# Kernel optimization log

Measured on AMD Instinct MI355X. Metric: run time of the kernel, lower is better.

## Reference

```python
import jax, jax.numpy as jnp
import numpy as np

EPS = 1e-5


def conv1x1(x, w, b):
    # x: [b,c,h,w], w: [o,c], b: [o] -> [b,o,h,w]  (1x1 conv == channel matmul)
    return jnp.einsum('bchw,oc->bohw', x, w) + b[None, :, None, None]


def nor_mean_std(x):
    # instance norm over spatial dims (torch calc_mean_std uses unbiased var)
    mean = jnp.mean(x, axis=(2, 3), keepdims=True)
    var = jnp.var(x, axis=(2, 3), keepdims=True, ddof=1)
    return (x - mean) / jnp.sqrt(var + EPS)


def nor_mean(x):
    mean = jnp.mean(x, axis=(2, 3), keepdims=True)
    return x - mean, mean


def net(x, w1, b1, w2, b2):
    return conv1x1(jax.nn.relu(conv1x1(x, w1, b1)), w2, b2)


def setup_inputs() -> dict:
    key = jax.random.key(0)
    ks = jax.random.split(key, 8)
    B, C, H, W = 8, 256, 128, 128
    return {
        'content': jax.random.normal(ks[0], (B, C, H, W), jnp.float32),
        'style': jax.random.normal(ks[1], (B, C, H, W), jnp.float32),
        'w1': jax.random.normal(ks[2], (128, 256), jnp.float32) * 0.05,
        'b1': jax.random.normal(ks[3], (128,), jnp.float32) * 0.05,
        'w2': jax.random.normal(ks[4], (32, 128), jnp.float32) * 0.05,
        'b2': jax.random.normal(ks[5], (32,), jnp.float32) * 0.05,
        'wu': jax.random.normal(ks[6], (256, 32), jnp.float32) * 0.05,
        'bu': jax.random.normal(ks[7], (256,), jnp.float32) * 0.05,
    }


def reference(content, style, w1, b1, w2, b2, wu, bu):
    cF_nor = nor_mean_std(content)
    sF_nor, smean = nor_mean(style)
    cF = net(cF_nor, w1, b1, w2, b2)          # [b,32,h,w]
    sF = net(sF_nor, w1, b1, w2, b2)          # [b,32,h,w]
    b, c, h, w = cF.shape
    hw = h * w
    sf = sF.reshape(b, c, hw)
    # channel covariance: [b,32,32]
    s_cov = jnp.einsum('bcn,bdn->bcd', sf, sf) / hw
    s_cov = jax.nn.softmax(s_cov, axis=-1) * (c ** -0.5)
    gF = jnp.einsum('bcd,bdn->bcn', s_cov, cF.reshape(b, c, hw)).reshape(b, c, h, w)
    gF = conv1x1(gF, wu, bu)                  # [b,256,h,w]
    return gF + smean + content
```

## Files before the change

### kernel.cpp

```cpp
#include <hip/hip_runtime.h>

#define HW 16384
#define C_IN 256
#define C_MID 128
#define C_OUT 32
#define EPSF 1e-5f

typedef __bf16 bf16x8 __attribute__((ext_vector_type(8)));
typedef __bf16 bf16x4 __attribute__((ext_vector_type(4)));
typedef float f32x4 __attribute__((ext_vector_type(4)));

__device__ __forceinline__ bf16x4 cvt4(f32x4 v) {
    bf16x4 r;
    r[0] = (__bf16)v[0]; r[1] = (__bf16)v[1];
    r[2] = (__bf16)v[2]; r[3] = (__bf16)v[3];
    return r;
}

template <int MODE>
__global__ __launch_bounds__(512) void k_stats8(const float* __restrict__ content,
                                                const float* __restrict__ style,
                                                float* __restrict__ cmean,
                                                float* __restrict__ crstd,
                                                float* __restrict__ smean,
                                                __bf16* __restrict__ cbf,
                                                __bf16* __restrict__ sbf) {
    const int bc = blockIdx.x;
    const int t = threadIdx.x;
    const f32x4* cp = (const f32x4*)(content + (size_t)bc * HW);
    const f32x4* sp = (const f32x4*)(style + (size_t)bc * HW);
    const int phase = (bc * 257) & 4095;

    int idx[8];
    #pragma unroll
    for (int i = 0; i < 8; ++i) idx[i] = (phase + t + i * 512) & 4095;

    f32x4 c[8], s[8];
    #pragma unroll
    for (int i = 0; i < 8; ++i)
        c[i] = (MODE == 1) ? __builtin_nontemporal_load(cp + idx[i]) : cp[idx[i]];
    #pragma unroll
    for (int i = 0; i < 8; ++i)
        s[i] = __builtin_nontemporal_load(sp + idx[i]);
    asm volatile("" ::
        "v"(c[0]), "v"(c[1]), "v"(c[2]), "v"(c[3]), "v"(c[4]), "v"(c[5]), "v"(c[6]), "v"(c[7]),
        "v"(s[0]), "v"(s[1]), "v"(s[2]), "v"(s[3]), "v"(s[4]), "v"(s[5]), "v"(s[6]), "v"(s[7]));

    if constexpr (MODE == 1) {
        bf16x4* cb = (bf16x4*)(cbf + (size_t)bc * HW);
        bf16x4* sb = (bf16x4*)(sbf + (size_t)bc * HW);
        #pragma unroll
        for (int i = 0; i < 8; ++i) {
            cb[idx[i]] = cvt4(c[i]);
            sb[idx[i]] = cvt4(s[i]);
        }
    }

    float cs, cq, ss;
    {
        f32x4 a01 = c[0] + c[1], a23 = c[2] + c[3], a45 = c[4] + c[5], a67 = c[6] + c[7];
        f32x4 a = (a01 + a23) + (a45 + a67);
        cs = (a[0] + a[1]) + (a[2] + a[3]);
        f32x4 q01 = c[0]*c[0] + c[1]*c[1], q23 = c[2]*c[2] + c[3]*c[3];
        f32x4 q45 = c[4]*c[4] + c[5]*c[5], q67 = c[6]*c[6] + c[7]*c[7];
        f32x4 q = (q01 + q23) + (q45 + q67);
        cq = (q[0] + q[1]) + (q[2] + q[3]);
        f32x4 b01 = s[0] + s[1], b23 = s[2] + s[3], b45 = s[4] + s[5], b67 = s[6] + s[7];
        f32x4 bsum = (b01 + b23) + (b45 + b67);
        ss = (bsum[0] + bsum[1]) + (bsum[2] + bsum[3]);
    }

    #pragma unroll
    for (int d = 32; d > 0; d >>= 1) {
        cs += __shfl_xor(cs, d, 64);
        cq += __shfl_xor(cq, d, 64);
        ss += __shfl_xor(ss, d, 64);
    }
    __shared__ float rs[8], rq[8], rss[8];
    const int wv = t >> 6;
    if ((t & 63) == 0) { rs[wv] = cs; rq[wv] = cq; rss[wv] = ss; }
    __syncthreads();
    if (t == 0) {
        float S = 0.f, Q = 0.f, SS = 0.f;
        #pragma unroll
        for (int i = 0; i < 8; ++i) { S += rs[i]; Q += rq[i]; SS += rss[i]; }
        float n = (float)HW;
        float var = (Q - S * S / n) / (n - 1.f);
        cmean[bc] = S / n;
        crstd[bc] = 1.f / sqrtf(var + EPSF);
        smean[bc] = SS / n;
    }
}

__global__ __launch_bounds__(256) void k_wprep(const float* __restrict__ w1,
                                               const float* __restrict__ b1,
                                               const float* __restrict__ cmean,
                                               const float* __restrict__ crstd,
                                               const float* __restrict__ smean,
                                               __bf16* __restrict__ W1c,
                                               float* __restrict__ bias1c,
                                               __bf16* __restrict__ W1s,
                                               float* __restrict__ bias1s) {
    int o = blockIdx.x, b = blockIdx.y, t = threadIdx.x;
    float w = w1[o * 256 + t];
    float r = crstd[b * 256 + t];
    float wc = w * r;
    W1c[((size_t)(b * 128 + o)) * 256 + t] = (__bf16)wc;
    if (b == 0) W1s[o * 256 + t] = (__bf16)w;
    float pc = wc * cmean[b * 256 + t];
    float ps = w * smean[b * 256 + t];
    __shared__ float rA[256], rB[256];
    rA[t] = pc; rB[t] = ps;
    __syncthreads();
    for (int off = 128; off > 0; off >>= 1) {
        if (t < off) { rA[t] += rA[t + off]; rB[t] += rB[t + off]; }
        __syncthreads();
    }
    if (t == 0) {
        bias1c[b * 128 + o] = b1[o] - rA[0];
        bias1s[b * 128 + o] = b1[o] - rB[0];
    }
}

__global__ __launch_bounds__(256) void k_w2prep(const float* __restrict__ w2,
                                                __bf16* __restrict__ W2b) {
    int i = blockIdx.x * 256 + threadIdx.x;
    if (i < 4096) W2b[i] = (__bf16)w2[i];
}

template <bool NT>
__device__ __forceinline__ float ld_f32(const float* p) {
    if constexpr (NT) return __builtin_nontemporal_load(p);
    else return *p;
}

template <bool NT_X>
__global__ __launch_bounds__(256) void k_net_mfma(const float* __restrict__ x,
                                                  const __bf16* __restrict__ W1,
                                                  const float* __restrict__ bias1,
                                                  const __bf16* __restrict__ W2,
                                                  const float* __restrict__ b2,
                                                  float* __restrict__ outF,
                                                  int w1_per_batch) {
    __shared__ __bf16 Xl[64 * 256];
    __shared__ __bf16 Tl[64 * 128];
    const int tid = threadIdx.x;
    const int l = tid & 63, wv = tid >> 6;
    const int lr = l & 15, g = l >> 4;
    const int sw = (lr & 7) << 4;
    const int p0 = blockIdx.x * 64;
    const int b = blockIdx.y;
    const float* xb = x + (size_t)b * C_IN * HW;

    {
        const int p = wv * 16 + lr;
        const float* xp = xb + p0 + p;
        char* row = (char*)&Xl[p * 256];
        #pragma unroll 4
        for (int cc = 0; cc < 16; ++cc) {
            const int c = cc * 16 + g * 4;
            float f0 = ld_f32<NT_X>(xp + (size_t)(c + 0) * HW);
            float f1 = ld_f32<NT_X>(xp + (size_t)(c + 1) * HW);
            float f2 = ld_f32<NT_X>(xp + (size_t)(c + 2) * HW);
            float f3 = ld_f32<NT_X>(xp + (size_t)(c + 3) * HW);
            bf16x4 v;
            v[0] = (__bf16)f0; v[1] = (__bf16)f1; v[2] = (__bf16)f2; v[3] = (__bf16)f3;
            *(bf16x4*)(row + ((c * 2) ^ sw)) = v;
        }
    }
    __syncthreads();

    const f32x4 zero4 = {0.f, 0.f, 0.f, 0.f};
    f32x4 acc[2][4];
    #pragma unroll
    for (int mt = 0; mt < 2; ++mt)
        #pragma unroll
        for (int nt = 0; nt < 4; ++nt) acc[mt][nt] = zero4;

    const __bf16* W1b = W1 + (w1_per_batch ? ((size_t)b << 15) : 0);
    const __bf16* wrow0 = W1b + (size_t)(wv * 32 + lr) * 256 + g * 8;
    const __bf16* wrow1 = wrow0 + 16 * 256;

    #pragma unroll
    for (int kt = 0; kt < 8; ++kt) {
        bf16x8 a0 = *(const bf16x8*)(wrow0 + kt * 32);
        bf16x8 a1 = *(const bf16x8*)(wrow1 + kt * 32);
        #pragma unroll
        for (int nt = 0; nt < 4; ++nt) {
            const char* xrow = (const char*)&Xl[(nt * 16 + lr) * 256];
            bf16x8 bfr = *(const bf16x8*)(xrow + (((kt * 32 + g * 8) * 2) ^ sw));
            acc[0][nt] = __builtin_amdgcn_mfma_f32_16x16x32_bf16(a0, bfr, acc[0][nt], 0, 0, 0);
            acc[1][nt] = __builtin_amdgcn_mfma_f32_16x16x32_bf16(a1, bfr, acc[1][nt], 0, 0, 0);
        }
    }

    float4 bia[2];
    bia[0] = *(const float4*)&bias1[b * 128 + wv * 32 + g * 4];
    bia[1] = *(const float4*)&bias1[b * 128 + wv * 32 + 16 + g * 4];
    #pragma unroll
    for (int mt = 0; mt < 2; ++mt) {
        #pragma unroll
        for (int nt = 0; nt < 4; ++nt) {
            const int p = nt * 16 + lr;
            char* trow = (char*)&Tl[p * 128];
            const int ob = (wv * 32 + mt * 16 + g * 4) * 2;
            bf16x4 tv;
            tv[0] = (__bf16)fmaxf(acc[mt][nt][0] + bia[mt].x, 0.f);
            tv[1] = (__bf16)fmaxf(acc[mt][nt][1] + bia[mt].y, 0.f);
            tv[2] = (__bf16)fmaxf(acc[mt][nt][2] + bia[mt].z, 0.f);
            tv[3] = (__bf16)fmaxf(acc[mt][nt][3] + bia[mt].w, 0.f);
            *(bf16x4*)(trow + (ob ^ sw)) = tv;
        }
    }
    __syncthreads();

    f32x4 acc2[2];
    acc2[0] = zero4; acc2[1] = zero4;
    const int p = wv * 16 + lr;
    const char* trow = (const char*)&Tl[p * 128];
    const __bf16* w2r0 = W2 + (size_t)lr * 128 + g * 8;
    const __bf16* w2r1 = w2r0 + 16 * 128;
    #pragma unroll
    for (int kt = 0; kt < 4; ++kt) {
        bf16x8 bfr = *(const bf16x8*)(trow + (((kt * 32 + g * 8) * 2) ^ sw));
        bf16x8 a0 = *(const bf16x8*)(w2r0 + kt * 32);
        bf16x8 a1 = *(const bf16x8*)(w2r1 + kt * 32);
        acc2[0] = __builtin_amdgcn_mfma_f32_16x16x32_bf16(a0, bfr, acc2[0], 0, 0, 0);
        acc2[1] = __builtin_amdgcn_mfma_f32_16x16x32_bf16(a1, bfr, acc2[1], 0, 0, 0);
    }
    float4 bb0 = *(const float4*)&b2[g * 4];
    float4 bb1 = *(const float4*)&b2[16 + g * 4];
    float* ob = outF + (size_t)b * C_OUT * HW + p0 + p;
    const int o0 = g * 4;
    ob[(size_t)(o0 + 0) * HW] = acc2[0][0] + bb0.x;
    ob[(size_t)(o0 + 1) * HW] = acc2[0][1] + bb0.y;
    ob[(size_t)(o0 + 2) * HW] = acc2[0][2] + bb0.z;
    ob[(size_t)(o0 + 3) * HW] = acc2[0][3] + bb0.w;
    ob[(size_t)(16 + o0 + 0) * HW] = acc2[1][0] + bb1.x;
    ob[(size_t)(16 + o0 + 1) * HW] = acc2[1][1] + bb1.y;
    ob[(size_t)(16 + o0 + 2) * HW] = acc2[1][2] + bb1.z;
    ob[(size_t)(16 + o0 + 3) * HW] = acc2[1][3] + bb1.w;
}

__global__ __launch_bounds__(256) void k_net_mfma_bf(const __bf16* __restrict__ x,
                                                     const __bf16* __restrict__ W1,
                                                     const float* __restrict__ bias1,
                                                     const __bf16* __restrict__ W2,
                                                     const float* __restrict__ b2,
                                                     float* __restrict__ outF,
                                                     int w1_per_batch) {
    __shared__ __bf16 Xl[64 * 256];
    __shared__ __bf16 Tl[64 * 128];
    const int tid = threadIdx.x;
    const int l = tid & 63, wv = tid >> 6;
    const int lr = l & 15, g = l >> 4;
    const int sw = (lr & 7) << 4;
    const int p0 = blockIdx.x * 64;
    const int b = blockIdx.y;
    const __bf16* xb = x + (size_t)b * C_IN * HW;

    {
        const int p = wv * 16 + lr;
        const __bf16* xp = xb + p0 + p;
        char* row = (char*)&Xl[p * 256];
        #pragma unroll 4
        for (int cc = 0; cc < 16; ++cc) {
            const int c = cc * 16 + g * 4;
            bf16x4 v;
            v[0] = xp[(size_t)(c + 0) * HW];
            v[1] = xp[(size_t)(c + 1) * HW];
            v[2] = xp[(size_t)(c + 2) * HW];
            v[3] = xp[(size_t)(c + 3) * HW];
            *(bf16x4*)(row + ((c * 2) ^ sw)) = v;
        }
    }
    __syncthreads();

    const f32x4 zero4 = {0.f, 0.f, 0.f, 0.f};
    f32x4 acc[2][4];
    #pragma unroll
    for (int mt = 0; mt < 2; ++mt)
        #pragma unroll
        for (int nt = 0; nt < 4; ++nt) acc[mt][nt] = zero4;

    const __bf16* W1b = W1 + (w1_per_batch ? ((size_t)b << 15) : 0);
    const __bf16* wrow0 = W1b + (size_t)(wv * 32 + lr) * 256 + g * 8;
    const __bf16* wrow1 = wrow0 + 16 * 256;

    #pragma unroll
    for (int kt = 0; kt < 8; ++kt) {
        bf16x8 a0 = *(const bf16x8*)(wrow0 + kt * 32);
        bf16x8 a1 = *(const bf16x8*)(wrow1 + kt * 32);
        #pragma unroll
        for (int nt = 0; nt < 4; ++nt) {
            const char* xrow = (const char*)&Xl[(nt * 16 + lr) * 256];
            bf16x8 bfr = *(const bf16x8*)(xrow + (((kt * 32 + g * 8) * 2) ^ sw));
            acc[0][nt] = __builtin_amdgcn_mfma_f32_16x16x32_bf16(a0, bfr, acc[0][nt], 0, 0, 0);
            acc[1][nt] = __builtin_amdgcn_mfma_f32_16x16x32_bf16(a1, bfr, acc[1][nt], 0, 0, 0);
        }
    }

    float4 bia[2];
    bia[0] = *(const float4*)&bias1[b * 128 + wv * 32 + g * 4];
    bia[1] = *(const float4*)&bias1[b * 128 + wv * 32 + 16 + g * 4];
    #pragma unroll
    for (int mt = 0; mt < 2; ++mt) {
        #pragma unroll
        for (int nt = 0; nt < 4; ++nt) {
            const int p = nt * 16 + lr;
            char* trow = (char*)&Tl[p * 128];
            const int ob = (wv * 32 + mt * 16 + g * 4) * 2;
            bf16x4 tv;
            tv[0] = (__bf16)fmaxf(acc[mt][nt][0] + bia[mt].x, 0.f);
            tv[1] = (__bf16)fmaxf(acc[mt][nt][1] + bia[mt].y, 0.f);
            tv[2] = (__bf16)fmaxf(acc[mt][nt][2] + bia[mt].z, 0.f);
            tv[3] = (__bf16)fmaxf(acc[mt][nt][3] + bia[mt].w, 0.f);
            *(bf16x4*)(trow + (ob ^ sw)) = tv;
        }
    }
    __syncthreads();

    f32x4 acc2[2];
    acc2[0] = zero4; acc2[1] = zero4;
    const int p = wv * 16 + lr;
    const char* trow = (const char*)&Tl[p * 128];
    const __bf16* w2r0 = W2 + (size_t)lr * 128 + g * 8;
    const __bf16* w2r1 = w2r0 + 16 * 128;
    #pragma unroll
    for (int kt = 0; kt < 4; ++kt) {
        bf16x8 bfr = *(const bf16x8*)(trow + (((kt * 32 + g * 8) * 2) ^ sw));
        bf16x8 a0 = *(const bf16x8*)(w2r0 + kt * 32);
        bf16x8 a1 = *(const bf16x8*)(w2r1 + kt * 32);
        acc2[0] = __builtin_amdgcn_mfma_f32_16x16x32_bf16(a0, bfr, acc2[0], 0, 0, 0);
        acc2[1] = __builtin_amdgcn_mfma_f32_16x16x32_bf16(a1, bfr, acc2[1], 0, 0, 0);
    }
    float4 bb0 = *(const float4*)&b2[g * 4];
    float4 bb1 = *(const float4*)&b2[16 + g * 4];
    float* ob = outF + (size_t)b * C_OUT * HW + p0 + p;
    const int o0 = g * 4;
    ob[(size_t)(o0 + 0) * HW] = acc2[0][0] + bb0.x;
    ob[(size_t)(o0 + 1) * HW] = acc2[0][1] + bb0.y;
    ob[(size_t)(o0 + 2) * HW] = acc2[0][2] + bb0.z;
    ob[(size_t)(o0 + 3) * HW] = acc2[0][3] + bb0.w;
    ob[(size_t)(16 + o0 + 0) * HW] = acc2[1][0] + bb1.x;
    ob[(size_t)(16 + o0 + 1) * HW] = acc2[1][1] + bb1.y;
    ob[(size_t)(16 + o0 + 2) * HW] = acc2[1][2] + bb1.z;
    ob[(size_t)(16 + o0 + 3) * HW] = acc2[1][3] + bb1.w;
}

__global__ __launch_bounds__(256) void k_gram(const float* __restrict__ sF,
                                              float* __restrict__ partial) {
    __shared__ float sS[32 * 257];
    int b = blockIdx.y, sl = blockIdx.x;
    int t = threadIdx.x;
    const float* base = sF + (size_t)b * C_OUT * HW + sl * 1024;
    int i = t >> 3, jb = (t & 7) * 4;
    float acc[4] = {0.f, 0.f, 0.f, 0.f};
    for (int ch = 0; ch < 4; ++ch) {
        __syncthreads();
        #pragma unroll
        for (int r = 0; r < 32; ++r)
            sS[r * 257 + t] = base[(size_t)r * HW + ch * 256 + t];
        __syncthreads();
        for (int n = 0; n < 256; ++n) {
            float si = sS[i * 257 + n];
            #pragma unroll
            for (int q = 0; q < 4; ++q)
                acc[q] = fmaf(si, sS[(jb + q) * 257 + n], acc[q]);
        }
    }
    float* dst = partial + ((size_t)(b * 16 + sl)) * 1024 + t * 4;
    #pragma unroll
    for (int q = 0; q < 4; ++q) dst[q] = acc[q];
}

__global__ __launch_bounds__(1024) void k_softmax(const float* __restrict__ partial,
                                                  float* __restrict__ scov) {
    int b = blockIdx.x;
    int j = threadIdx.x, i = threadIdx.y;
    float v = 0.f;
    #pragma unroll
    for (int s = 0; s < 16; ++s)
        v += partial[((size_t)(b * 16 + s)) * 1024 + i * 32 + j];
    v *= (1.f / (float)HW);
    float m = v;
    #pragma unroll
    for (int d = 16; d > 0; d >>= 1) m = fmaxf(m, __shfl_xor(m, d, 32));
    float e = expf(v - m);
    float sum = e;
    #pragma unroll
    for (int d = 16; d > 0; d >>= 1) sum += __shfl_xor(sum, d, 32);
    scov[(size_t)b * 1024 + i * 32 + j] = e / sum * 0.17677669529663687f;
}

template <bool CONTENT_BF16>
__global__ __launch_bounds__(256) void k_final(const float* __restrict__ cF,
                                               const float* __restrict__ scov,
                                               const float* __restrict__ wu,
                                               const float* __restrict__ bu,
                                               const float* __restrict__ smean,
                                               const float* __restrict__ content,
                                               const __bf16* __restrict__ cbf,
                                               float* __restrict__ out) {
    __shared__ float sCov[1024];
    __shared__ float sC[32 * 64];
    __shared__ float sG[32 * 64];
    __shared__ float sWu[32 * 260];
    int t = threadIdx.x;
    int p0 = blockIdx.x * 64;
    int b = blockIdx.y;
    #pragma unroll
    for (int q = 0; q < 4; ++q) sCov[t + 256 * q] = scov[(size_t)b * 1024 + t + 256 * q];
    {
        int p = t & 63, rb = t >> 6;
        #pragma unroll
        for (int pass = 0; pass < 8; ++pass) {
            int r = pass * 4 + rb;
            sC[r * 64 + p] = cF[(size_t)b * C_OUT * HW + (size_t)r * HW + p0 + p];
        }
    }
    {
        int k = t & 31, ob = t >> 5;
        #pragma unroll
        for (int pass = 0; pass < 32; ++pass) {
            int o = pass * 8 + ob;
            sWu[k * 260 + o] = wu[o * 32 + k];
        }
    }
    __syncthreads();
    {
        int gp = t & 63, gib = (t >> 6) * 8;
        #pragma unroll
        for (int rr = 0; rr < 8; ++rr) {
            int gi = gib + rr;
            float a = 0.f;
            #pragma unroll
            for (int k = 0; k < 32; ++k)
                a = fmaf(sCov[gi * 32 + k], sC[k * 64 + gp], a);
            sG[gi * 64 + gp] = a;
        }
    }
    __syncthreads();
    int tx = t & 7, ty = t >> 3;
    float acc[8][8];
    #pragma unroll
    for (int i = 0; i < 8; ++i)
        #pragma unroll
        for (int j = 0; j < 8; ++j) acc[i][j] = 0.f;
    #pragma unroll 4
    for (int k = 0; k < 32; ++k) {
        float4 a4a = *(const float4*)&sWu[k * 260 + ty * 8];
        float4 a4b = *(const float4*)&sWu[k * 260 + ty * 8 + 4];
        float4 b4a = *(const float4*)&sG[k * 64 + tx * 8];
        float4 b4b = *(const float4*)&sG[k * 64 + tx * 8 + 4];
        float a[8] = {a4a.x, a4a.y, a4a.z, a4a.w, a4b.x, a4b.y, a4b.z, a4b.w};
        float bb[8] = {b4a.x, b4a.y, b4a.z, b4a.w, b4b.x, b4b.y, b4b.z, b4b.w};
        #pragma unroll
        for (int i = 0; i < 8; ++i)
            #pragma unroll
            for (int j = 0; j < 8; ++j)
                acc[i][j] = fmaf(a[i], bb[j], acc[i][j]);
    }
    #pragma unroll
    for (int i = 0; i < 8; ++i) {
        int o = ty * 8 + i;
        float add = bu[o] + smean[b * 256 + o];
        float* dst = out + (size_t)b * C_IN * HW + (size_t)o * HW + p0 + tx * 8;
        float cv[8];
        if constexpr (CONTENT_BF16) {
            const __bf16* csrc = cbf + (size_t)b * C_IN * HW + (size_t)o * HW + p0 + tx * 8;
            bf16x8 cvv = *(const bf16x8*)csrc;
            #pragma unroll
            for (int q = 0; q < 8; ++q) cv[q] = (float)cvv[q];
        } else {
            const float* csrc = content + (size_t)b * C_IN * HW + (size_t)o * HW + p0 + tx * 8;
            float4 c0 = *(const float4*)csrc;
            float4 c1 = *(const float4*)(csrc + 4);
            cv[0] = c0.x; cv[1] = c0.y; cv[2] = c0.z; cv[3] = c0.w;
            cv[4] = c1.x; cv[5] = c1.y; cv[6] = c1.z; cv[7] = c1.w;
        }
        f32x4 r0 = {acc[i][0] + add + cv[0], acc[i][1] + add + cv[1],
                    acc[i][2] + add + cv[2], acc[i][3] + add + cv[3]};
        f32x4 r1 = {acc[i][4] + add + cv[4], acc[i][5] + add + cv[5],
                    acc[i][6] + add + cv[6], acc[i][7] + add + cv[7]};
        __builtin_nontemporal_store(r0, (f32x4*)dst);
        __builtin_nontemporal_store(r1, (f32x4*)(dst + 4));
    }
}

extern "C" void kernel_launch(void* const* d_in, const int* in_sizes, int n_in,
                              void* d_out, int out_size, void* d_ws, size_t ws_size,
                              hipStream_t stream) {
    const float* content = (const float*)d_in[0];
    const float* style   = (const float*)d_in[1];
    const float* w1      = (const float*)d_in[2];
    const float* b1      = (const float*)d_in[3];
    const float* w2      = (const float*)d_in[4];
    const float* b2      = (const float*)d_in[5];
    const float* wu      = (const float*)d_in[6];
    const float* bu      = (const float*)d_in[7];
    float* out = (float*)d_out;
    float* ws  = (float*)d_ws;

    const size_t NEED = 42240000ull * sizeof(float);
    if (ws_size >= NEED) {
        float* cmean   = ws;
        float* crstd   = ws + 2048;
        float* smean   = ws + 4096;
        float* scov    = ws + 6144;
        float* bias1c  = ws + 14336;
        float* bias1s  = ws + 15360;
        __bf16* W2b    = (__bf16*)(ws + 16384);
        __bf16* W1s    = (__bf16*)(ws + 18432);
        __bf16* W1c    = (__bf16*)(ws + 34816);
        float* partial = ws + 165888;
        float* cF      = ws + 296960;
        float* sF      = cF + 4194304;
        __bf16* cbf    = (__bf16*)(ws + 8685568);
        __bf16* sbf    = (__bf16*)(ws + 8685568 + 16777216);

        k_stats8<1><<<dim3(2048), 512, 0, stream>>>(content, style, cmean, crstd, smean, cbf, sbf);
        k_wprep<<<dim3(128, 8), 256, 0, stream>>>(w1, b1, cmean, crstd, smean,
                                                  W1c, bias1c, W1s, bias1s);
        k_w2prep<<<dim3(16), 256, 0, stream>>>(w2, W2b);
        k_net_mfma_bf<<<dim3(256, 8), 256, 0, stream>>>(cbf, W1c, bias1c, W2b, b2, cF, 1);
        k_net_mfma_bf<<<dim3(256, 8), 256, 0, stream>>>(sbf, W1s, bias1s, W2b, b2, sF, 0);
        k_gram<<<dim3(16, 8), 256, 0, stream>>>(sF, partial);
        k_softmax<<<dim3(8), dim3(32, 32), 0, stream>>>(partial, scov);
        k_final<true><<<dim3(256, 8), 256, 0, stream>>>(cF, scov, wu, bu, smean,
                                                        content, cbf, out);
    } else {
        float* cmean   = ws;
        float* crstd   = ws + 2048;
        float* smean   = ws + 4096;
        float* scov    = ws + 6144;
        __bf16* W2b    = (__bf16*)(ws + 6144);
        float* bias1c  = ws + 8192;
        float* bias1s  = ws + 9216;
        float* partial = ws + 14336;
        __bf16* W1c    = (__bf16*)(ws + 14336);
        __bf16* W1s    = (__bf16*)(ws + 145408);
        float* cF      = ws + 161792;
        float* sF      = cF + 4194304;

        k_stats8<0><<<dim3(2048), 512, 0, stream>>>(content, style, cmean, crstd, smean,
                                                    nullptr, nullptr);
        k_wprep<<<dim3(128, 8), 256, 0, stream>>>(w1, b1, cmean, crstd, smean,
                                                  W1c, bias1c, W1s, bias1s);
        k_w2prep<<<dim3(16), 256, 0, stream>>>(w2, W2b);
        k_net_mfma<false><<<dim3(256, 8), 256, 0, stream>>>(content, W1c, bias1c, W2b, b2, cF, 1);
        k_net_mfma<true><<<dim3(256, 8), 256, 0, stream>>>(style, W1s, bias1s, W2b, b2, sF, 0);
        k_gram<<<dim3(16, 8), 256, 0, stream>>>(sF, partial);
        k_softmax<<<dim3(8), dim3(32, 32), 0, stream>>>(partial, scov);
        k_final<false><<<dim3(256, 8), 256, 0, stream>>>(cF, scov, wu, bu, smean,
                                                         content, nullptr, out);
    }
}
```

Measured before the change: 246.3 us.

## Drop bf16 content copy, read fp32 content directly, fold w2 prep into wprep

The stats kernel no longer writes a bf16 copy of content; only style is converted to bf16. The content net pass reads fp32 content directly (hoping for cache hits after stats), and the final kernel reads fp32 content for the residual instead of the bf16 copy, which also removes the bf16 rounding of the residual. The separate w2 conversion kernel is merged into the weight-prep kernel. The final kernel reads wu directly from global/cache instead of staging it in shared memory. This trades a 32MB write for extra fp32 reads.

```diff
diff --git a/kernel.cpp b/kernel.cpp
--- a/kernel.cpp
+++ b/kernel.cpp
@@ -17,13 +17,11 @@
     return r;
 }
 
-template <int MODE>
-__global__ __launch_bounds__(512) void k_stats8(const float* __restrict__ content,
+__global__ __launch_bounds__(512) void k_stats9(const float* __restrict__ content,
                                                 const float* __restrict__ style,
                                                 float* __restrict__ cmean,
                                                 float* __restrict__ crstd,
                                                 float* __restrict__ smean,
-                                                __bf16* __restrict__ cbf,
                                                 __bf16* __restrict__ sbf) {
     const int bc = blockIdx.x;
     const int t = threadIdx.x;
@@ -37,23 +35,17 @@
 
     f32x4 c[8], s[8];
     #pragma unroll
-    for (int i = 0; i < 8; ++i)
-        c[i] = (MODE == 1) ? __builtin_nontemporal_load(cp + idx[i]) : cp[idx[i]];
-    #pragma unroll
-    for (int i = 0; i < 8; ++i)
-        s[i] = __builtin_nontemporal_load(sp + idx[i]);
+    for (int i = 0; i < 8; ++i) c[i] = cp[idx[i]];
+    #pragma unroll
+    for (int i = 0; i < 8; ++i) s[i] = __builtin_nontemporal_load(sp + idx[i]);
     asm volatile("" ::
         "v"(c[0]), "v"(c[1]), "v"(c[2]), "v"(c[3]), "v"(c[4]), "v"(c[5]), "v"(c[6]), "v"(c[7]),
         "v"(s[0]), "v"(s[1]), "v"(s[2]), "v"(s[3]), "v"(s[4]), "v"(s[5]), "v"(s[6]), "v"(s[7]));
 
-    if constexpr (MODE == 1) {
-        bf16x4* cb = (bf16x4*)(cbf + (size_t)bc * HW);
+    {
         bf16x4* sb = (bf16x4*)(sbf + (size_t)bc * HW);
         #pragma unroll
-        for (int i = 0; i < 8; ++i) {
-            cb[idx[i]] = cvt4(c[i]);
-            sb[idx[i]] = cvt4(s[i]);
-        }
+        for (int i = 0; i < 8; ++i) sb[idx[i]] = cvt4(s[i]);
     }
 
     float cs, cq, ss;
@@ -92,21 +84,26 @@
     }
 }
 
-__global__ __launch_bounds__(256) void k_wprep(const float* __restrict__ w1,
-                                               const float* __restrict__ b1,
-                                               const float* __restrict__ cmean,
-                                               const float* __restrict__ crstd,
-                                               const float* __restrict__ smean,
-                                               __bf16* __restrict__ W1c,
-                                               float* __restrict__ bias1c,
-                                               __bf16* __restrict__ W1s,
-                                               float* __restrict__ bias1s) {
+__global__ __launch_bounds__(256) void k_wprep2(const float* __restrict__ w1,
+                                                const float* __restrict__ b1,
+                                                const float* __restrict__ w2,
+                                                const float* __restrict__ cmean,
+                                                const float* __restrict__ crstd,
+                                                const float* __restrict__ smean,
+                                                __bf16* __restrict__ W1c,
+                                                float* __restrict__ bias1c,
+                                                __bf16* __restrict__ W1s,
+                                                float* __restrict__ bias1s,
+                                                __bf16* __restrict__ W2b) {
     int o = blockIdx.x, b = blockIdx.y, t = threadIdx.x;
     float w = w1[o * 256 + t];
     float r = crstd[b * 256 + t];
     float wc = w * r;
     W1c[((size_t)(b * 128 + o)) * 256 + t] = (__bf16)wc;
-    if (b == 0) W1s[o * 256 + t] = (__bf16)w;
+    if (b == 0) {
+        W1s[o * 256 + t] = (__bf16)w;
+        if (t < 32) W2b[o * 32 + t] = (__bf16)w2[o * 32 + t];
+    }
     float pc = wc * cmean[b * 256 + t];
     float ps = w * smean[b * 256 + t];
     __shared__ float rA[256], rB[256];
@@ -122,19 +119,6 @@
     }
 }
 
-__global__ __launch_bounds__(256) void k_w2prep(const float* __restrict__ w2,
-                                                __bf16* __restrict__ W2b) {
-    int i = blockIdx.x * 256 + threadIdx.x;
-    if (i < 4096) W2b[i] = (__bf16)w2[i];
-}
-
-template <bool NT>
-__device__ __forceinline__ float ld_f32(const float* p) {
-    if constexpr (NT) return __builtin_nontemporal_load(p);
-    else return *p;
-}
-
-template <bool NT_X>
 __global__ __launch_bounds__(256) void k_net_mfma(const float* __restrict__ x,
                                                   const __bf16* __restrict__ W1,
                                                   const float* __restrict__ bias1,
@@ -159,10 +143,10 @@
         #pragma unroll 4
         for (int cc = 0; cc < 16; ++cc) {
             const int c = cc * 16 + g * 4;
-            float f0 = ld_f32<NT_X>(xp + (size_t)(c + 0) * HW);
-            float f1 = ld_f32<NT_X>(xp + (size_t)(c + 1) * HW);
-            float f2 = ld_f32<NT_X>(xp + (size_t)(c + 2) * HW);
-            float f3 = ld_f32<NT_X>(xp + (size_t)(c + 3) * HW);
+            float f0 = xp[(size_t)(c + 0) * HW];
+            float f1 = xp[(size_t)(c + 1) * HW];
+            float f2 = xp[(size_t)(c + 2) * HW];
+            float f3 = xp[(size_t)(c + 3) * HW];
             bf16x4 v;
             v[0] = (__bf16)f0; v[1] = (__bf16)f1; v[2] = (__bf16)f2; v[3] = (__bf16)f3;
             *(bf16x4*)(row + ((c * 2) ^ sw)) = v;
@@ -393,19 +377,16 @@
     scov[(size_t)b * 1024 + i * 32 + j] = e / sum * 0.17677669529663687f;
 }
 
-template <bool CONTENT_BF16>
-__global__ __launch_bounds__(256) void k_final(const float* __restrict__ cF,
-                                               const float* __restrict__ scov,
-                                               const float* __restrict__ wu,
-                                               const float* __restrict__ bu,
-                                               const float* __restrict__ smean,
-                                               const float* __restrict__ content,
-                                               const __bf16* __restrict__ cbf,
-                                               float* __restrict__ out) {
+__global__ __launch_bounds__(256) void k_final2(const float* __restrict__ cF,
+                                                const float* __restrict__ scov,
+                                                const float* __restrict__ wu,
+                                                const float* __restrict__ bu,
+                                                const float* __restrict__ smean,
+                                                const float* __restrict__ content,
+                                                float* __restrict__ out) {
     __shared__ float sCov[1024];
     __shared__ float sC[32 * 64];
     __shared__ float sG[32 * 64];
-    __shared__ float sWu[32 * 260];
     int t = threadIdx.x;
     int p0 = blockIdx.x * 64;
     int b = blockIdx.y;
@@ -417,14 +398,6 @@
         for (int pass = 0; pass < 8; ++pass) {
             int r = pass * 4 + rb;
             sC[r * 64 + p] = cF[(size_t)b * C_OUT * HW + (size_t)r * HW + p0 + p];
-        }
-    }
-    {
-        int k = t & 31, ob = t >> 5;
-        #pragma unroll
-        for (int pass = 0; pass < 32; ++pass) {
-            int o = pass * 8 + ob;
-            sWu[k * 260 + o] = wu[o * 32 + k];
         }
     }
     __syncthreads();
@@ -442,6 +415,7 @@
     }
     __syncthreads();
     int tx = t & 7, ty = t >> 3;
+    const float* wurow = wu + (size_t)(ty * 8) * 32;
     float acc[8][8];
     #pragma unroll
     for (int i = 0; i < 8; ++i)
@@ -449,11 +423,11 @@
         for (int j = 0; j < 8; ++j) acc[i][j] = 0.f;
     #pragma unroll 4
     for (int k = 0; k < 32; ++k) {
-        float4 a4a = *(const float4*)&sWu[k * 260 + ty * 8];
-        float4 a4b = *(const float4*)&sWu[k * 260 + ty * 8 + 4];
+        float a[8];
+        #pragma unroll
+        for (int i = 0; i < 8; ++i) a[i] = wurow[i * 32 + k];
         float4 b4a = *(const float4*)&sG[k * 64 + tx * 8];
         float4 b4b = *(const float4*)&sG[k * 64 + tx * 8 + 4];
-        float a[8] = {a4a.x, a4a.y, a4a.z, a4a.w, a4b.x, a4b.y, a4b.z, a4b.w};
         float bb[8] = {b4a.x, b4a.y, b4a.z, b4a.w, b4b.x, b4b.y, b4b.z, b4b.w};
         #pragma unroll
         for (int i = 0; i < 8; ++i)
@@ -465,24 +439,14 @@
     for (int i = 0; i < 8; ++i) {
         int o = ty * 8 + i;
         float add = bu[o] + smean[b * 256 + o];
+        const float* csrc = content + (size_t)b * C_IN * HW + (size_t)o * HW + p0 + tx * 8;
         float* dst = out + (size_t)b * C_IN * HW + (size_t)o * HW + p0 + tx * 8;
-        float cv[8];
-        if constexpr (CONTENT_BF16) {
-            const __bf16* csrc = cbf + (size_t)b * C_IN * HW + (size_t)o * HW + p0 + tx * 8;
-            bf16x8 cvv = *(const bf16x8*)csrc;
-            #pragma unroll
-            for (int q = 0; q < 8; ++q) cv[q] = (float)cvv[q];
-        } else {
-            const float* csrc = content + (size_t)b * C_IN * HW + (size_t)o * HW + p0 + tx * 8;
-            float4 c0 = *(const float4*)csrc;
-            float4 c1 = *(const float4*)(csrc + 4);
-            cv[0] = c0.x; cv[1] = c0.y; cv[2] = c0.z; cv[3] = c0.w;
-            cv[4] = c1.x; cv[5] = c1.y; cv[6] = c1.z; cv[7] = c1.w;
-        }
-        f32x4 r0 = {acc[i][0] + add + cv[0], acc[i][1] + add + cv[1],
-                    acc[i][2] + add + cv[2], acc[i][3] + add + cv[3]};
-        f32x4 r1 = {acc[i][4] + add + cv[4], acc[i][5] + add + cv[5],
-                    acc[i][6] + add + cv[6], acc[i][7] + add + cv[7]};
+        float4 c0 = *(const float4*)csrc;
+        float4 c1 = *(const float4*)(csrc + 4);
+        f32x4 r0 = {acc[i][0] + add + c0.x, acc[i][1] + add + c0.y,
+                    acc[i][2] + add + c0.z, acc[i][3] + add + c0.w};
+        f32x4 r1 = {acc[i][4] + add + c1.x, acc[i][5] + add + c1.y,
+                    acc[i][6] + add + c1.z, acc[i][7] + add + c1.w};
         __builtin_nontemporal_store(r0, (f32x4*)dst);
         __builtin_nontemporal_store(r1, (f32x4*)(dst + 4));
     }
@@ -502,57 +466,26 @@
     float* out = (float*)d_out;
     float* ws  = (float*)d_ws;
 
-    const size_t NEED = 42240000ull * sizeof(float);
-    if (ws_size >= NEED) {
-        float* cmean   = ws;
-        float* crstd   = ws + 2048;
-        float* smean   = ws + 4096;
-        float* scov    = ws + 6144;
-        float* bias1c  = ws + 14336;
-        float* bias1s  = ws + 15360;
-        __bf16* W2b    = (__bf16*)(ws + 16384);
-        __bf16* W1s    = (__bf16*)(ws + 18432);
-        __bf16* W1c    = (__bf16*)(ws + 34816);
-        float* partial = ws + 165888;
-        float* cF      = ws + 296960;
-        float* sF      = cF + 4194304;
-        __bf16* cbf    = (__bf16*)(ws + 8685568);
-        __bf16* sbf    = (__bf16*)(ws + 8685568 + 16777216);
-
-        k_stats8<1><<<dim3(2048), 512, 0, stream>>>(content, style, cmean, crstd, smean, cbf, sbf);
-        k_wprep<<<dim3(128, 8), 256, 0, stream>>>(w1, b1, cmean, crstd, smean,
-                                                  W1c, bias1c, W1s, bias1s);
-        k_w2prep<<<dim3(16), 256, 0, stream>>>(w2, W2b);
-        k_net_mfma_bf<<<dim3(256, 8), 256, 0, stream>>>(cbf, W1c, bias1c, W2b, b2, cF, 1);
-        k_net_mfma_bf<<<dim3(256, 8), 256, 0, stream>>>(sbf, W1s, bias1s, W2b, b2, sF, 0);
-        k_gram<<<dim3(16, 8), 256, 0, stream>>>(sF, partial);
-        k_softmax<<<dim3(8), dim3(32, 32), 0, stream>>>(partial, scov);
-        k_final<true><<<dim3(256, 8), 256, 0, stream>>>(cF, scov, wu, bu, smean,
-                                                        content, cbf, out);
-    } else {
-        float* cmean   = ws;
-        float* crstd   = ws + 2048;
-        float* smean   = ws + 4096;
-        float* scov    = ws + 6144;
-        __bf16* W2b    = (__bf16*)(ws + 6144);
-        float* bias1c  = ws + 8192;
-        float* bias1s  = ws + 9216;
-        float* partial = ws + 14336;
-        __bf16* W1c    = (__bf16*)(ws + 14336);
-        __bf16* W1s    = (__bf16*)(ws + 145408);
-        float* cF      = ws + 161792;
-        float* sF      = cF + 4194304;
-
-        k_stats8<0><<<dim3(2048), 512, 0, stream>>>(content, style, cmean, crstd, smean,
-                                                    nullptr, nullptr);
-        k_wprep<<<dim3(128, 8), 256, 0, stream>>>(w1, b1, cmean, crstd, smean,
-                                                  W1c, bias1c, W1s, bias1s);
-        k_w2prep<<<dim3(16), 256, 0, stream>>>(w2, W2b);
-        k_net_mfma<false><<<dim3(256, 8), 256, 0, stream>>>(content, W1c, bias1c, W2b, b2, cF, 1);
-        k_net_mfma<true><<<dim3(256, 8), 256, 0, stream>>>(style, W1s, bias1s, W2b, b2, sF, 0);
-        k_gram<<<dim3(16, 8), 256, 0, stream>>>(sF, partial);
-        k_softmax<<<dim3(8), dim3(32, 32), 0, stream>>>(partial, scov);
-        k_final<false><<<dim3(256, 8), 256, 0, stream>>>(cF, scov, wu, bu, smean,
-                                                         content, nullptr, out);
-    }
-}
+    float* cmean   = ws;
+    float* crstd   = ws + 2048;
+    float* smean   = ws + 4096;
+    float* scov    = ws + 6144;
+    float* bias1c  = ws + 14336;
+    float* bias1s  = ws + 15360;
+    __bf16* W2b    = (__bf16*)(ws + 16384);
+    __bf16* W1s    = (__bf16*)(ws + 18432);
+    __bf16* W1c    = (__bf16*)(ws + 34816);
+    float* partial = ws + 165888;
+    float* cF      = ws + 296960;
+    float* sF      = cF + 4194304;
+    __bf16* sbf    = (__bf16*)(ws + 8685568);
+
+    k_stats9<<<dim3(2048), 512, 0, stream>>>(content, style, cmean, crstd, smean, sbf);
+    k_wprep2<<<dim3(128, 8), 256, 0, stream>>>(w1, b1, w2, cmean, crstd, smean,
+                                               W1c, bias1c, W1s, bias1s, W2b);
+    k_net_mfma<<<dim3(256, 8), 256, 0, stream>>>(content, W1c, bias1c, W2b, b2, cF, 1);
+    k_net_mfma_bf<<<dim3(256, 8), 256, 0, stream>>>(sbf, W1s, bias1s, W2b, b2, sF, 0);
+    k_gram<<<dim3(16, 8), 256, 0, stream>>>(sF, partial);
+    k_softmax<<<dim3(8), dim3(32, 32), 0, stream>>>(partial, scov);
+    k_final2<<<dim3(256, 8), 256, 0, stream>>>(cF, scov, wu, bu, smean, content, out);
+}
```

After: 253.1 us. 2.8% more time.
